# Kernel tuning notes

Hardware: AMD Instinct MI355X
Metric: run time of the kernel (lower is better)

The kernel has to match this reference:

```python
import math
import jax, jax.numpy as jnp
import numpy as np

TAU = 0.07
GROUPS = 8
COST_CH = 96

def _l2norm(x, axis, eps=1e-12):
    # matches torch F.normalize: x / max(||x||_2, eps)
    n = jnp.sqrt(jnp.sum(x * x, axis=axis, keepdims=True))
    return x / jnp.maximum(n, eps)

def setup_inputs() -> dict:
    key = jax.random.key(0)
    k0, k1, k2, k3 = jax.random.split(key, 4)
    B, Cin, H, W = 2, 64, 128, 256
    F_L = jax.random.normal(k0, (B, Cin, H, W), jnp.float32)
    F_R = jax.random.normal(k1, (B, Cin, H, W), jnp.float32)
    WL = jax.random.normal(k2, (COST_CH, Cin), jnp.float32) * 0.1  # pL 1x1 conv weight
    WR = jax.random.normal(k3, (COST_CH, Cin), jnp.float32) * 0.1  # pR 1x1 conv weight
    return {"F_L": F_L, "F_R": F_R, "WL": WL, "WR": WR, "D_orig": 128}

def reference(F_L, F_R, WL, WR, D_orig):
    B, _, H, W = F_L.shape
    Dp = int(math.ceil(D_orig / 4.0))  # Dp_full; full band dmin=0, dmax=Dp-1
    # 1x1 conv projections + channel L2 normalize
    FL = _l2norm(jnp.einsum('bchw,oc->bohw', F_L, WL), axis=1)
    FR = _l2norm(jnp.einsum('bchw,oc->bohw', F_R, WR), axis=1)
    G, Cg = GROUPS, COST_CH // GROUPS
    disp = jnp.arange(Dp)
    # grid_sample(bilinear, border, align_corners=True) with integer disparity
    # shift == border-clamped integer gather along W: x' = clip(x - d, 0, W-1)
    idx = jnp.clip(jnp.arange(W)[None, :] - disp[:, None], 0, W - 1)  # [Dp, W]
    FRs = FR[:, :, :, idx]  # [B, C, H, Dp, W] warped right features
    FLg = FL.reshape(B, G, Cg, H, W)
    FRsg = FRs.reshape(B, G, Cg, H, Dp, W)
    # grouped correlation: reduce over Cg, scaled by 1/sqrt(Cg)
    sim = jnp.einsum('bgchw,bgchdw->bgdhw', FLg, FRsg) / jnp.sqrt(jnp.float32(Cg))
    # sin positional modulation
    psi = jnp.sin(2.0 * jnp.pi * disp.astype(FL.dtype) / max(Dp, 1))
    cost = -(sim + psi[None, None, :, None, None]) / TAU  # [B, G, Dp, H, W]
    return cost
```

## Files before the change

kernel.cpp:

```cpp
#include <hip/hip_runtime.h>
#include <math.h>

#define TAU_F 0.07f
#define B_ 2
#define CIN 64
#define H_ 128
#define W_ 256
#define CC 96
#define G_ 8
#define CG 12
#define DP 32
#define HW_ (H_*W_)
#define ROWF (W_*CG)

__global__ void wtrans_kernel(const float* __restrict__ WL,
                              const float* __restrict__ WR,
                              float* __restrict__ WtL,
                              float* __restrict__ WtR) {
    int i = blockIdx.x * 256 + threadIdx.x;
    if (i >= 2 * CIN * CC) return;
    int side = i / (CIN * CC);
    int r = i % (CIN * CC);
    int c = r / CC;
    int o = r % CC;
    const float* src = side ? WR : WL;
    float* dst = side ? WtR : WtL;
    dst[r] = src[o * CIN + c];
}

__global__ __launch_bounds__(256, 4) void proj_kernel(
    const float* __restrict__ F_L, const float* __restrict__ F_R,
    const float* __restrict__ WtL, const float* __restrict__ WtR,
    float* __restrict__ outL, float* __restrict__ outR)
{
    __shared__ float ssS[256];

    const int blk  = blockIdx.x;
    const int side = blk & 1;
    const int wh   = (blk >> 1) & 1;
    const int h    = (blk >> 2) & 127;
    const int b    = blk >> 9;

    const int t    = threadIdx.x;
    const int half = t >> 7;
    const int wl   = t & 127;
    const int w    = wh * 128 + wl;

    const float* F  = side ? F_R : F_L;
    const float* Wt = side ? WtR : WtL;
    float* out      = side ? outR : outL;

    const int hoff = __builtin_amdgcn_readfirstlane(half * 48);
    const float* WtU = Wt + hoff;

    float y[48];
#pragma unroll
    for (int k = 0; k < 48; ++k) y[k] = 0.f;

    const float* fp = F + (size_t)b * CIN * HW_ + h * W_ + wh * 128 + wl;

#pragma unroll 4
    for (int c = 0; c < CIN; ++c) {
        float f = fp[c * HW_];
        const float* wr = WtU + c * CC;
#pragma unroll
        for (int k = 0; k < 48; ++k) y[k] = fmaf(f, wr[k], y[k]);
    }

    float ss = 0.f;
#pragma unroll
    for (int k = 0; k < 48; ++k) ss = fmaf(y[k], y[k], ss);
    ssS[t] = ss;
    __syncthreads();
    float tot = ss + ssS[t ^ 128];
    float r = 1.0f / fmaxf(sqrtf(tot), 1e-12f);

    size_t base = (size_t)(b * H_ + h) * (G_ * ROWF);
#pragma unroll
    for (int gq = 0; gq < 4; ++gq) {
        int g = half * 4 + gq;
#pragma unroll
        for (int j = 0; j < 3; ++j) {
            float4 v;
            v.x = y[gq*12 + j*4 + 0] * r;
            v.y = y[gq*12 + j*4 + 1] * r;
            v.z = y[gq*12 + j*4 + 2] * r;
            v.w = y[gq*12 + j*4 + 3] * r;
            *(float4*)&out[base + (size_t)g * ROWF + j * (W_*4) + w * 4] = v;
        }
    }
}

__global__ __launch_bounds__(256) void sim_kernel(
    const float* __restrict__ PL, const float* __restrict__ PR,
    float* __restrict__ out)
{
    __shared__ float flS[ROWF];
    __shared__ float frS[ROWF];
    __shared__ float psiS[DP];

    int blk = blockIdx.x;
    int h = blk % H_;
    int g = (blk / H_) % G_;
    int b = blk / (H_ * G_);
    int tid = threadIdx.x;

    size_t base = ((size_t)(b * H_ + h) * G_ + g) * ROWF;

#pragma unroll
    for (int i = tid; i < ROWF / 4; i += 256) {
        *(float4*)&flS[i * 4] = *(const float4*)&PL[base + (size_t)i * 4];
        *(float4*)&frS[i * 4] = *(const float4*)&PR[base + (size_t)i * 4];
    }
    if (tid < DP)
        psiS[tid] = -sinf(6.28318530717958647692f * (float)tid / (float)DP) / TAU_F;
    __syncthreads();

    const int w = tid;
    float4 fl0 = *(const float4*)&flS[0*1024 + w*4];
    float4 fl1 = *(const float4*)&flS[1*1024 + w*4];
    float4 fl2 = *(const float4*)&flS[2*1024 + w*4];

    const float A = -1.0f / (3.46410161513775459f * TAU_F);
    size_t ob = ((size_t)(b * G_ + g) * DP * H_ + h) * W_ + w;

#pragma unroll
    for (int d = 0; d < DP; ++d) {
        int wd = w - d; if (wd < 0) wd = 0;
        float4 a0 = *(const float4*)&frS[0*1024 + wd*4];
        float4 a1 = *(const float4*)&frS[1*1024 + wd*4];
        float4 a2 = *(const float4*)&frS[2*1024 + wd*4];
        float acc;
        acc = fl0.x * a0.x;
        acc = fmaf(fl0.y, a0.y, acc);
        acc = fmaf(fl0.z, a0.z, acc);
        acc = fmaf(fl0.w, a0.w, acc);
        acc = fmaf(fl1.x, a1.x, acc);
        acc = fmaf(fl1.y, a1.y, acc);
        acc = fmaf(fl1.z, a1.z, acc);
        acc = fmaf(fl1.w, a1.w, acc);
        acc = fmaf(fl2.x, a2.x, acc);
        acc = fmaf(fl2.y, a2.y, acc);
        acc = fmaf(fl2.z, a2.z, acc);
        acc = fmaf(fl2.w, a2.w, acc);
        out[ob + (size_t)d * HW_] = fmaf(acc, A, psiS[d]);
    }
}

extern "C" void kernel_launch(void* const* d_in, const int* in_sizes, int n_in,
                              void* d_out, int out_size, void* d_ws, size_t ws_size,
                              hipStream_t stream) {
    const float* F_L = (const float*)d_in[0];
    const float* F_R = (const float*)d_in[1];
    const float* WL  = (const float*)d_in[2];
    const float* WR  = (const float*)d_in[3];
    float* out = (float*)d_out;
    float* ws  = (float*)d_ws;

    const size_t PROJ = (size_t)B_ * H_ * G_ * ROWF;
    float* PLp = ws;
    float* PRp = ws + PROJ;
    float* WtL = ws + 2 * PROJ;
    float* WtR = WtL + CIN * CC;

    wtrans_kernel<<<(2 * CIN * CC + 255) / 256, 256, 0, stream>>>(WL, WR, WtL, WtR);
    proj_kernel<<<dim3(B_ * H_ * 2 * 2), 256, 0, stream>>>(F_L, F_R, WtL, WtR, PLp, PRp);
    sim_kernel<<<B_ * G_ * H_, 256, 0, stream>>>(PLp, PRp, out);
}
```

Before: 131.9 us.

## Register-block four output columns per thread with sliding window of right features

The sim kernel now gives each wavefront one (b,g,h) row, with each lane computing four adjacent w positions. It keeps a rotating four-entry register window of right features, so each disparity step needs only one new 48-byte shared load instead of three per output. Left features are read straight from global into registers, right features go into an XOR-swizzled LDS layout to reduce bank conflicts, and outputs are written as float4. This cuts LDS traffic and gives wider stores, at the cost of higher register pressure (launch bounds 256,3) and four times fewer blocks.

```diff
diff --git a/kernel.cpp b/kernel.cpp
--- a/kernel.cpp
+++ b/kernel.cpp
@@ -91,59 +91,99 @@
     }
 }
 
-__global__ __launch_bounds__(256) void sim_kernel(
+__global__ __launch_bounds__(256, 3) void sim_kernel(
     const float* __restrict__ PL, const float* __restrict__ PR,
     float* __restrict__ out)
 {
-    __shared__ float flS[ROWF];
-    __shared__ float frS[ROWF];
+    __shared__ float frS[4 * ROWF];
     __shared__ float psiS[DP];
 
-    int blk = blockIdx.x;
-    int h = blk % H_;
-    int g = (blk / H_) % G_;
-    int b = blk / (H_ * G_);
-    int tid = threadIdx.x;
-
-    size_t base = ((size_t)(b * H_ + h) * G_ + g) * ROWF;
-
-#pragma unroll
-    for (int i = tid; i < ROWF / 4; i += 256) {
-        *(float4*)&flS[i * 4] = *(const float4*)&PL[base + (size_t)i * 4];
-        *(float4*)&frS[i * 4] = *(const float4*)&PR[base + (size_t)i * 4];
-    }
+    const int tid = threadIdx.x;
+    const int wv  = tid >> 6;
+    const int l   = tid & 63;
+    const int row = (blockIdx.x << 2) | wv;
+    const int h = row % H_;
+    const int g = (row / H_) % G_;
+    const int b = row / (H_ * G_);
+
     if (tid < DP)
         psiS[tid] = -sinf(6.28318530717958647692f * (float)tid / (float)DP) / TAU_F;
+
+    const size_t base = ((size_t)(b * H_ + h) * G_ + g) * ROWF;
+    const float* PRrow = PR + base;
+    const float* PLrow = PL + base;
+    char* frW = (char*)&frS[wv * ROWF];
+
+#pragma unroll
+    for (int j = 0; j < 3; ++j) {
+#pragma unroll
+        for (int i = 0; i < 4; ++i) {
+            int w = 4 * l + i;
+            float4 v = *(const float4*)&PRrow[j * 1024 + w * 4];
+            int byt = j * 4096 + w * 16;
+            byt ^= ((byt >> 7) & 7) << 4;
+            *(float4*)(frW + byt) = v;
+        }
+    }
+
+    float4 fl[4][3];
+#pragma unroll
+    for (int i = 0; i < 4; ++i)
+#pragma unroll
+        for (int j = 0; j < 3; ++j)
+            fl[i][j] = *(const float4*)&PLrow[j * 1024 + (4 * l + i) * 4];
+
     __syncthreads();
 
-    const int w = tid;
-    float4 fl0 = *(const float4*)&flS[0*1024 + w*4];
-    float4 fl1 = *(const float4*)&flS[1*1024 + w*4];
-    float4 fl2 = *(const float4*)&flS[2*1024 + w*4];
+    float4 wnd[4][3];
+#pragma unroll
+    for (int i = 0; i < 4; ++i) {
+#pragma unroll
+        for (int j = 0; j < 3; ++j) {
+            int byt = j * 4096 + (4 * l + i) * 16;
+            byt ^= ((byt >> 7) & 7) << 4;
+            wnd[i][j] = *(const float4*)(frW + byt);
+        }
+    }
 
     const float A = -1.0f / (3.46410161513775459f * TAU_F);
-    size_t ob = ((size_t)(b * G_ + g) * DP * H_ + h) * W_ + w;
+    const size_t ob = (((size_t)(b * G_ + g) * DP) * H_ + h) * (size_t)W_ + 4 * l;
 
 #pragma unroll
     for (int d = 0; d < DP; ++d) {
-        int wd = w - d; if (wd < 0) wd = 0;
-        float4 a0 = *(const float4*)&frS[0*1024 + wd*4];
-        float4 a1 = *(const float4*)&frS[1*1024 + wd*4];
-        float4 a2 = *(const float4*)&frS[2*1024 + wd*4];
-        float acc;
-        acc = fl0.x * a0.x;
-        acc = fmaf(fl0.y, a0.y, acc);
-        acc = fmaf(fl0.z, a0.z, acc);
-        acc = fmaf(fl0.w, a0.w, acc);
-        acc = fmaf(fl1.x, a1.x, acc);
-        acc = fmaf(fl1.y, a1.y, acc);
-        acc = fmaf(fl1.z, a1.z, acc);
-        acc = fmaf(fl1.w, a1.w, acc);
-        acc = fmaf(fl2.x, a2.x, acc);
-        acc = fmaf(fl2.y, a2.y, acc);
-        acc = fmaf(fl2.z, a2.z, acc);
-        acc = fmaf(fl2.w, a2.w, acc);
-        out[ob + (size_t)d * HW_] = fmaf(acc, A, psiS[d]);
+        const float p = psiS[d];
+        float r[4];
+#pragma unroll
+        for (int i = 0; i < 4; ++i) {
+            const int s = (i - d) & 3;
+            float acc;
+            acc = fl[i][0].x * wnd[s][0].x;
+            acc = fmaf(fl[i][0].y, wnd[s][0].y, acc);
+            acc = fmaf(fl[i][0].z, wnd[s][0].z, acc);
+            acc = fmaf(fl[i][0].w, wnd[s][0].w, acc);
+            acc = fmaf(fl[i][1].x, wnd[s][1].x, acc);
+            acc = fmaf(fl[i][1].y, wnd[s][1].y, acc);
+            acc = fmaf(fl[i][1].z, wnd[s][1].z, acc);
+            acc = fmaf(fl[i][1].w, wnd[s][1].w, acc);
+            acc = fmaf(fl[i][2].x, wnd[s][2].x, acc);
+            acc = fmaf(fl[i][2].y, wnd[s][2].y, acc);
+            acc = fmaf(fl[i][2].z, wnd[s][2].z, acc);
+            acc = fmaf(fl[i][2].w, wnd[s][2].w, acc);
+            r[i] = fmaf(acc, A, p);
+        }
+        *(float4*)&out[ob + (size_t)d * HW_] = make_float4(r[0], r[1], r[2], r[3]);
+
+        if (d < DP - 1) {
+            int wd = 4 * l - (d + 1); if (wd < 0) wd = 0;
+            const int s = (-(d + 1)) & 3;
+            const int byt0 = wd * 16;
+#pragma unroll
+            for (int j = 0; j < 3; ++j) {
+                int byt = j * 4096 + byt0;
+                byt ^= ((byt >> 7) & 7) << 4;
+                wnd[s][j] = *(const float4*)(frW + byt);
+            }
+        }
     }
 }
 
@@ -165,5 +205,5 @@
 
     wtrans_kernel<<<(2 * CIN * CC + 255) / 256, 256, 0, stream>>>(WL, WR, WtL, WtR);
     proj_kernel<<<dim3(B_ * H_ * 2 * 2), 256, 0, stream>>>(F_L, F_R, WtL, WtR, PLp, PRp);
-    sim_kernel<<<B_ * G_ * H_, 256, 0, stream>>>(PLp, PRp, out);
-}
+    sim_kernel<<<(B_ * G_ * H_) / 4, 256, 0, stream>>>(PLp, PRp, out);
+}
```

Result: no change. 134.4 us (+1.9%).
